# Optimization experiments

Hardware: AMD Instinct MI355X
Metric: run time of the kernel (lower is better)

## Reference

```python
import jax, jax.numpy as jnp
import numpy as np

B, S, F, H = 2, 2048, 2048, 16
DH = F // H  # head_dim = 128
ROPE_BASE = 10000.0


def apply_rope(x, offset):
    # x: [B, S, H, Dh]; rotate-half RoPE per head with positions offset..offset+S-1
    d = x.shape[-1]
    pos = jnp.arange(x.shape[1], dtype=jnp.float32) + offset          # [S]
    inv_freq = 1.0 / (ROPE_BASE ** (jnp.arange(0, d, 2, dtype=jnp.float32) / d))  # [Dh/2]
    ang = pos[:, None] * inv_freq[None, :]                             # [S, Dh/2]
    cos = jnp.cos(ang)[None, :, None, :].astype(x.dtype)               # [1,S,1,Dh/2]
    sin = jnp.sin(ang)[None, :, None, :].astype(x.dtype)
    x1, x2 = x[..., : d // 2], x[..., d // 2 :]
    return jnp.concatenate([x1 * cos - x2 * sin, x1 * sin + x2 * cos], axis=-1)


def setup_inputs() -> dict:
    key = jax.random.key(0)
    k0, k1, k2, k3 = jax.random.split(key, 4)
    lecun = (1.0 / F) ** 0.5
    in_q = jax.random.normal(k0, (B, S, F), dtype=jnp.float32)
    Wq = jax.random.normal(k1, (F, H, DH), dtype=jnp.float32) * lecun
    Wk = jax.random.normal(k2, (F, H, DH), dtype=jnp.float32) * lecun
    Wv = jax.random.normal(k3, (F, H, DH), dtype=jnp.float32) * lecun
    bq = jnp.zeros((H, DH), dtype=jnp.float32)
    bk = jnp.zeros((H, DH), dtype=jnp.float32)
    bv = jnp.zeros((H, DH), dtype=jnp.float32)
    mask = jnp.tril(jnp.ones((S, S), dtype=bool))[None, None, :, :]  # causal [1,1,S,S]
    return {"in_q": in_q, "Wq": Wq, "bq": bq, "Wk": Wk, "bk": bk,
            "Wv": Wv, "bv": bv, "mask": mask, "offset": 0}


def reference(in_q, Wq, bq, Wk, bk, Wv, bv, mask, offset):
    # QKV projections: LinearGeneral [B,S,F] x [F,H,Dh] -> [B,S,H,Dh]
    q = jnp.einsum("bsf,fhd->bshd", in_q, Wq) + bq
    k = jnp.einsum("bsf,fhd->bshd", in_q, Wk) + bk
    v = jnp.einsum("bsf,fhd->bshd", in_q, Wv) + bv
    # RoPE on q and k (merge/split-head reshape in original is a no-op on values)
    q = apply_rope(q, offset)
    k = apply_rope(k, offset)
    # dot-product attention
    scale = 1.0 / jnp.sqrt(jnp.asarray(DH, dtype=q.dtype))
    scores = jnp.einsum("bqhd,bkhd->bhqk", q, k) * scale   # [B,H,Sq,Skv]
    scores = jnp.where(mask, scores, jnp.finfo(scores.dtype).min)
    weights = jax.nn.softmax(scores, axis=-1)
    out = jnp.einsum("bhqk,bkhd->bqhd", weights, v)        # [B,S,H,Dh]
    return out.reshape(out.shape[0], out.shape[1], H * DH)  # merge heads
```

## Files before the change

### kernel.cpp

```cpp
#include <hip/hip_runtime.h>
#include <hip/hip_bf16.h>
#include <stdint.h>

#define NB 2
#define NS 2048
#define NFE 2048
#define NH 16
#define NDH 128

#define QSCALE (0.08838834764831845f * 1.4426950408889634f)

typedef __attribute__((ext_vector_type(4))) float f32x4;
typedef __attribute__((ext_vector_type(8))) __bf16 bf16x8;

__device__ __forceinline__ uint16_t f2bf(float f) {
  uint32_t u = __builtin_bit_cast(uint32_t, f);
  return (uint16_t)((u + 0x7fffu + ((u >> 16) & 1u)) >> 16);
}

__device__ __forceinline__ void gload_lds16(const void* g, void* l) {
  __builtin_amdgcn_global_load_lds((const __attribute__((address_space(1))) void*)g,
                                   (__attribute__((address_space(3))) void*)l,
                                   16, 0, 0);
}

#define MFMA16(a, b, c) __builtin_amdgcn_mfma_f32_16x16x32_bf16(a, b, c, 0, 0, 0)

__global__ void k_convert(const float* __restrict__ x, uint16_t* __restrict__ y) {
  int i = (blockIdx.x * 256 + threadIdx.x) * 4;
  float4 v = *(const float4*)(x + i);
  ushort4 o;
  o.x = f2bf(v.x); o.y = f2bf(v.y); o.z = f2bf(v.z); o.w = f2bf(v.w);
  *(ushort4*)(y + i) = o;
}

__global__ void k_wt(const float* __restrict__ Wq, const float* __restrict__ Wk,
                     const float* __restrict__ Wv, uint16_t* __restrict__ Wt) {
  int which = blockIdx.z;
  const float* Wsrc = (which == 0) ? Wq : ((which == 1) ? Wk : Wv);
  int k0 = blockIdx.x * 64, n0 = blockIdx.y * 64;
  __shared__ uint16_t tile[64][65];
  int t = threadIdx.x;
#pragma unroll
  for (int it = 0; it < 4; ++it) {
    int vec = t + it * 256;
    int r = vec >> 4, c4 = vec & 15;
    float4 v = *(const float4*)&Wsrc[(size_t)(k0 + r) * NFE + n0 + c4 * 4];
    tile[r][c4 * 4 + 0] = f2bf(v.x);
    tile[r][c4 * 4 + 1] = f2bf(v.y);
    tile[r][c4 * 4 + 2] = f2bf(v.z);
    tile[r][c4 * 4 + 3] = f2bf(v.w);
  }
  __syncthreads();
#pragma unroll
  for (int it = 0; it < 4; ++it) {
    int vec = t + it * 256;
    int r = vec >> 4, c4 = vec & 15;
    ushort4 o;
    o.x = tile[c4 * 4 + 0][r];
    o.y = tile[c4 * 4 + 1][r];
    o.z = tile[c4 * 4 + 2][r];
    o.w = tile[c4 * 4 + 3][r];
    *(ushort4*)&Wt[(size_t)which * NFE * NFE + (size_t)(n0 + r) * NFE + k0 + c4 * 4] = o;
  }
}

__global__ void k_rope_tab(float* __restrict__ cosT, float* __restrict__ sinT,
                           const int* __restrict__ offp) {
  int tid = blockIdx.x * 256 + threadIdx.x;
  int s = tid >> 6, i = tid & 63;
  float off = (float)offp[0];
  float inv = expf(-((float)i / 64.0f) * logf(10000.0f));
  float ang = ((float)s + off) * inv;
  cosT[tid] = cosf(ang);
  sinT[tid] = sinf(ang);
}

__global__ __launch_bounds__(512, 2) void k_gemm_qkv(
    const uint16_t* __restrict__ A, const uint16_t* __restrict__ Wt,
    const float* __restrict__ bq, const float* __restrict__ bk, const float* __restrict__ bv,
    const float* __restrict__ cosT, const float* __restrict__ sinT,
    uint16_t* __restrict__ qws, uint16_t* __restrict__ kws, uint16_t* __restrict__ vws) {
  __shared__ uint16_t SMEM[4][16384];

  int bid = blockIdx.x;
  int swzb = (bid & 7) * 48 + (bid >> 3);
  int bx = swzb & 15, by = swzb >> 4;
  int t = threadIdx.x, l = t & 63, w = t >> 6;
  int g = l >> 4, c = l & 15;
  int wr = w >> 1, wc = w & 1;

  int row0 = t >> 3;
  int swz = ((t & 7) ^ (row0 & 7)) << 3;
  const uint16_t* aTh = A + ((size_t)bx * 256 + row0) * NFE + swz;
  const uint16_t* bTh = Wt + ((size_t)by * 256 + row0) * NFE + swz;

#define STG(sbase, slot, h, kt)                                                   \
  do {                                                                            \
    const uint16_t* _s = (sbase) + (size_t)((h) * 128) * NFE + (size_t)(kt) * 64; \
    char* _d = (char*)(&SMEM[slot][0]) + (h) * 16384 + t * 16;                    \
    gload_lds16(_s, _d);                                                          \
    gload_lds16(_s + (size_t)64 * NFE, _d + 8192);                                \
  } while (0)

#define LDA_(buf, mh)                                                             \
  _Pragma("unroll") for (int mi = 0; mi < 2; ++mi)                                \
  _Pragma("unroll") for (int kk = 0; kk < 2; ++kk) {                              \
    int row = wr * 64 + ((mh) * 2 + mi) * 16 + c;                                 \
    af[mi][kk] = *(const bf16x8*)((const char*)SMEM[(buf) * 2] + row * 128 +      \
                                  (((kk * 4 + g) ^ (row & 7)) << 4));             \
  }

#define LDB_(buf, nh, BF)                                                         \
  _Pragma("unroll") for (int ni = 0; ni < 4; ++ni)                                \
  _Pragma("unroll") for (int kk = 0; kk < 2; ++kk) {                              \
    int row = wc * 128 + ((nh) * 4 + ni) * 16 + c;                                \
    BF[ni][kk] = *(const bf16x8*)((const char*)SMEM[(buf) * 2 + 1] + row * 128 +  \
                                  (((kk * 4 + g) ^ (row & 7)) << 4));             \
  }

#define MM_(mh, nh, BF)                                                           \
  _Pragma("unroll") for (int kk = 0; kk < 2; ++kk)                                \
  _Pragma("unroll") for (int mi = 0; mi < 2; ++mi)                                \
  _Pragma("unroll") for (int ni = 0; ni < 4; ++ni)                                \
    acc[(mh) * 2 + mi][(nh) * 4 + ni] =                                           \
        MFMA16(af[mi][kk], BF[ni][kk], acc[(mh) * 2 + mi][(nh) * 4 + ni]);

#define BAR_MID()                                          \
  do {                                                     \
    __builtin_amdgcn_s_barrier();                          \
    asm volatile("s_waitcnt lgkmcnt(0)" ::: "memory");     \
    __builtin_amdgcn_sched_barrier(0);                     \
    __builtin_amdgcn_s_setprio(1);                         \
  } while (0)
#define BAR_END()                                          \
  do {                                                     \
    __builtin_amdgcn_s_setprio(0);                         \
    __builtin_amdgcn_s_barrier();                          \
  } while (0)

  f32x4 acc[4][8];
#pragma unroll
  for (int m = 0; m < 4; ++m)
#pragma unroll
    for (int n = 0; n < 8; ++n) acc[m][n] = (f32x4){0.f, 0.f, 0.f, 0.f};

  bf16x8 af[2][2], bflo[4][2], bfhi[4][2];

  STG(aTh, 0, 0, 0); STG(aTh, 0, 1, 0); STG(bTh, 1, 0, 0); STG(bTh, 1, 1, 0);
  STG(aTh, 2, 0, 1); STG(aTh, 2, 1, 1); STG(bTh, 3, 0, 1); STG(bTh, 3, 1, 1);
  asm volatile("s_waitcnt vmcnt(8)" ::: "memory");
  __builtin_amdgcn_s_barrier();

  for (int i = 0; i < 15; ++i) {
    int t2 = 2 * i + 2, t3 = 2 * i + 3;
    LDA_(0, 0); LDB_(0, 0, bflo);
    BAR_MID(); MM_(0, 0, bflo); BAR_END();
    LDB_(0, 1, bfhi);
    BAR_MID(); MM_(0, 1, bfhi); BAR_END();
    LDA_(0, 1);
    STG(bTh, 1, 0, t2);
    BAR_MID(); MM_(1, 1, bfhi); BAR_END();
    STG(bTh, 1, 1, t2);
    asm volatile("s_waitcnt vmcnt(4)" ::: "memory");
    BAR_MID(); MM_(1, 0, bflo); BAR_END();
    LDA_(1, 0); LDB_(1, 0, bflo);
    STG(aTh, 0, 0, t2);
    BAR_MID(); MM_(0, 0, bflo); BAR_END();
    LDB_(1, 1, bfhi);
    STG(aTh, 0, 1, t2);
    BAR_MID(); MM_(0, 1, bfhi); BAR_END();
    LDA_(1, 1);
    STG(bTh, 3, 0, t3);
    BAR_MID(); MM_(1, 1, bfhi); BAR_END();
    STG(bTh, 3, 1, t3);
    STG(aTh, 2, 0, t3);
    STG(aTh, 2, 1, t3);
    asm volatile("s_waitcnt vmcnt(8)" ::: "memory");
    BAR_MID(); MM_(1, 0, bflo); BAR_END();
  }

  {
    LDA_(0, 0); LDB_(0, 0, bflo);
    BAR_MID(); MM_(0, 0, bflo); BAR_END();
    LDB_(0, 1, bfhi);
    BAR_MID(); MM_(0, 1, bfhi); BAR_END();
    LDA_(0, 1);
    BAR_MID(); MM_(1, 1, bfhi); BAR_END();
    asm volatile("s_waitcnt vmcnt(0)" ::: "memory");
    BAR_MID(); MM_(1, 0, bflo); BAR_END();
    LDA_(1, 0); LDB_(1, 0, bflo);
    BAR_MID(); MM_(0, 0, bflo); BAR_END();
    LDB_(1, 1, bfhi);
    BAR_MID(); MM_(0, 1, bfhi); BAR_END();
    LDA_(1, 1);
    BAR_MID(); MM_(1, 1, bfhi); BAR_END();
    BAR_MID(); MM_(1, 0, bflo); BAR_END();
  }

  int ghead = by * 2 + wc;
  int which = ghead >> 4, h = ghead & 15;
  const float* bias = (which == 0) ? bq : ((which == 1) ? bk : bv);
  uint16_t* outp = (which == 0) ? qws : ((which == 1) ? kws : vws);
  float scl = (which == 0) ? QSCALE : 1.0f;
  int mbase = bx * 256 + wr * 64;
  if (which < 2) {
#pragma unroll
    for (int m = 0; m < 4; ++m)
#pragma unroll
      for (int nf = 0; nf < 4; ++nf) {
        int i2 = nf * 16 + c;
        float b1 = bias[h * NDH + i2], b2 = bias[h * NDH + 64 + i2];
#pragma unroll
        for (int j = 0; j < 4; ++j) {
          int r = mbase + m * 16 + g * 4 + j;
          int bb = r >> 11, s = r & (NS - 1);
          float cs = cosT[(s << 6) + i2], sn = sinT[(s << 6) + i2];
          float x1 = acc[m][nf][j] + b1;
          float x2 = acc[m][nf + 4][j] + b2;
          uint16_t* op = outp + ((size_t)(bb * NH + h) * NS + s) * NDH;
          op[i2] = f2bf((x1 * cs - x2 * sn) * scl);
          op[64 + i2] = f2bf((x1 * sn + x2 * cs) * scl);
        }
      }
  } else {
#pragma unroll
    for (int m = 0; m < 4; ++m)
#pragma unroll
      for (int nf = 0; nf < 8; ++nf) {
        int d = nf * 16 + c;
        float bv_ = bias[h * NDH + d];
#pragma unroll
        for (int j = 0; j < 4; ++j) {
          int r = mbase + m * 16 + g * 4 + j;
          int bb = r >> 11, s = r & (NS - 1);
          outp[((size_t)(bb * NH + h) * NS + s) * NDH + d] = f2bf(acc[m][nf][j] + bv_);
        }
      }
  }
#undef STG
#undef LDA_
#undef LDB_
#undef MM_
#undef BAR_MID
#undef BAR_END
}

__global__ void k_vt(const uint16_t* __restrict__ v, uint16_t* __restrict__ vt) {
  int bh = blockIdx.z;
  int s0 = blockIdx.x * 64, d0 = blockIdx.y * 64;
  __shared__ uint16_t tile[64][65];
  int t = threadIdx.x;
#pragma unroll
  for (int it = 0; it < 4; ++it) {
    int vec = t + it * 256;
    int r = vec >> 4, c4 = vec & 15;
    ushort4 x = *(const ushort4*)&v[((size_t)bh * NS + s0 + r) * NDH + d0 + c4 * 4];
    tile[r][c4 * 4 + 0] = x.x;
    tile[r][c4 * 4 + 1] = x.y;
    tile[r][c4 * 4 + 2] = x.z;
    tile[r][c4 * 4 + 3] = x.w;
  }
  __syncthreads();
#pragma unroll
  for (int it = 0; it < 4; ++it) {
    int vec = t + it * 256;
    int r = vec >> 4, c4 = vec & 15;
    ushort4 o;
    o.x = tile[c4 * 4 + 0][r];
    o.y = tile[c4 * 4 + 1][r];
    o.z = tile[c4 * 4 + 2][r];
    o.w = tile[c4 * 4 + 3][r];
    *(ushort4*)&vt[((size_t)bh * NDH + d0 + r) * NS + s0 + c4 * 4] = o;
  }
}

__global__ __launch_bounds__(256, 4) void k_attn(
    const uint16_t* __restrict__ qws, const uint16_t* __restrict__ kws,
    const uint16_t* __restrict__ vtws, float* __restrict__ out) {
  __shared__ alignas(16) uint16_t Ksm[64 * 128];
  __shared__ alignas(16) uint16_t Vsm[128 * 64];
  __shared__ alignas(16) uint16_t Psm[4][16 * 64];

  int bh = blockIdx.x;
  int t = threadIdx.x, w = t >> 6, l = t & 63;
  int g = l >> 4, c = l & 15;
  int bb = bh >> 4, h = bh & 15;

  const uint16_t* Qp = qws + (size_t)bh * NS * NDH;
  const uint16_t* Kp = kws + (size_t)bh * NS * NDH;
  const uint16_t* Vp = vtws + (size_t)bh * NDH * NS;

  for (int pass = 0; pass < 2; ++pass) {
    int y64 = pass ? (31 - blockIdx.y) : blockIdx.y;
    int q0 = y64 * 64;
    int r = q0 + w * 16 + c;

    bf16x8 qf[4];
#pragma unroll
    for (int kk = 0; kk < 4; ++kk)
      qf[kk] = *(const bf16x8*)&Qp[(size_t)r * NDH + kk * 32 + g * 8];

    f32x4 acc_o[8];
    float mreg = -1e30f, lreg = 0.f;
#pragma unroll
    for (int n = 0; n < 8; ++n) acc_o[n] = (f32x4){0.f, 0.f, 0.f, 0.f};

    int nkt = y64 + 1;
    for (int kt = 0; kt < nkt; ++kt) {
#pragma unroll
      for (int cc = 0; cc < 4; ++cc) {
        int flat = cc * 256 + t;
        int row = flat >> 4, sub = flat & 15;
        int scol = ((sub ^ (row & 7)) << 3);
        gload_lds16(&Kp[(size_t)(kt * 64 + row) * NDH + scol], (char*)Ksm + flat * 16);
      }
#pragma unroll
      for (int cc = 0; cc < 4; ++cc) {
        int flat = cc * 256 + t;
        int row = flat >> 3, sub = flat & 7;
        int scol = ((sub ^ (row & 7)) << 3);
        gload_lds16(&Vp[(size_t)row * NS + kt * 64 + scol], (char*)Vsm + flat * 16);
      }
      __syncthreads();

      f32x4 sacc[4];
#pragma unroll
      for (int nf = 0; nf < 4; ++nf) sacc[nf] = (f32x4){0.f, 0.f, 0.f, 0.f};
#pragma unroll
      for (int kk = 0; kk < 4; ++kk) {
#pragma unroll
        for (int nf = 0; nf < 4; ++nf) {
          int row = nf * 16 + c;
          int kb = ((kk * 32 + g * 8) * 2) ^ ((row & 7) << 4);
          bf16x8 kfr = *(const bf16x8*)((const char*)Ksm + row * 256 + kb);
          sacc[nf] = MFMA16(kfr, qf[kk], sacc[nf]);
        }
      }

      if (kt == y64) {
#pragma unroll
        for (int nf = 0; nf < 4; ++nf)
#pragma unroll
          for (int j = 0; j < 4; ++j) {
            int kv = kt * 64 + nf * 16 + g * 4 + j;
            if (kv > r) sacc[nf][j] = -1e30f;
          }
      }

      float mx = -1e30f;
#pragma unroll
      for (int nf = 0; nf < 4; ++nf)
        mx = fmaxf(mx, fmaxf(fmaxf(sacc[nf][0], sacc[nf][1]),
                             fmaxf(sacc[nf][2], sacc[nf][3])));
      mx = fmaxf(mx, __shfl_xor(mx, 16));
      mx = fmaxf(mx, __shfl_xor(mx, 32));

      float mnew = mreg;
      if (!__all(mx <= mreg + 8.0f)) {
        mnew = fmaxf(mreg, mx);
        float alpha = exp2f(mreg - mnew);
        mreg = mnew;
        lreg *= alpha;
#pragma unroll
        for (int j = 0; j < 4; ++j) {
          float aj = __shfl(alpha, (l & 48) + g * 4 + j);
#pragma unroll
          for (int nf = 0; nf < 8; ++nf) acc_o[nf][j] *= aj;
        }
      }

      float rs = 0.f;
#pragma unroll
      for (int nf = 0; nf < 4; ++nf)
#pragma unroll
        for (int j = 0; j < 4; ++j) {
          float p = exp2f(sacc[nf][j] - mnew);
          sacc[nf][j] = p;
          rs += p;
        }
      rs += __shfl_xor(rs, 16);
      rs += __shfl_xor(rs, 32);
      lreg += rs;

#pragma unroll
      for (int nf = 0; nf < 4; ++nf) {
        uint32_t pk0 = (uint32_t)f2bf(sacc[nf][0]) | ((uint32_t)f2bf(sacc[nf][1]) << 16);
        uint32_t pk1 = (uint32_t)f2bf(sacc[nf][2]) | ((uint32_t)f2bf(sacc[nf][3]) << 16);
        int colb = (nf * 16 + g * 4) * 2;
        char* base = (char*)Psm[w] + c * 128;
        *(uint32_t*)(base + (colb ^ ((c & 7) << 4))) = pk0;
        *(uint32_t*)(base + ((colb + 4) ^ ((c & 7) << 4))) = pk1;
      }

#pragma unroll
      for (int kk2 = 0; kk2 < 2; ++kk2) {
        int prow = c;
        int pkb = ((kk2 * 32 + g * 8) * 2) ^ ((prow & 7) << 4);
        bf16x8 pf = *(const bf16x8*)((const char*)Psm[w] + prow * 128 + pkb);
#pragma unroll
        for (int nf = 0; nf < 8; ++nf) {
          int row = nf * 16 + c;
          int kb = ((kk2 * 32 + g * 8) * 2) ^ ((row & 7) << 4);
          bf16x8 vf = *(const bf16x8*)((const char*)Vsm + row * 128 + kb);
          acc_o[nf] = MFMA16(pf, vf, acc_o[nf]);
        }
      }
      __syncthreads();
    }

#pragma unroll
    for (int j = 0; j < 4; ++j) {
      float lj = __shfl(lreg, (l & 48) + g * 4 + j);
      float inv = 1.0f / lj;
      int s = q0 + w * 16 + g * 4 + j;
      float* op = out + ((size_t)(bb * NS + s)) * NFE + h * NDH;
#pragma unroll
      for (int nf = 0; nf < 8; ++nf) op[nf * 16 + c] = acc_o[nf][j] * inv;
    }
  }
}

extern "C" void kernel_launch(void* const* d_in, const int* in_sizes, int n_in,
                              void* d_out, int out_size, void* d_ws, size_t ws_size,
                              hipStream_t stream) {
  const float* in_q = (const float*)d_in[0];
  const float* Wq = (const float*)d_in[1];
  const float* bq = (const float*)d_in[2];
  const float* Wk = (const float*)d_in[3];
  const float* bk = (const float*)d_in[4];
  const float* Wv = (const float*)d_in[5];
  const float* bv = (const float*)d_in[6];
  const int* offp = (const int*)d_in[8];
  float* out = (float*)d_out;

  char* ws = (char*)d_ws;
  const size_t SZ_AQ = (size_t)4096 * 2048 * 2;
  const size_t SZ_WT = (size_t)3 * 2048 * 2048 * 2;
  const size_t SZ_TAB = (size_t)2048 * 64 * 4;
  const size_t SZ_QKV = (size_t)32 * 2048 * 128 * 2;
  uint16_t* Aq = (uint16_t*)(ws);
  uint16_t* Wt = (uint16_t*)(ws + SZ_AQ);
  float* cosT = (float*)(ws + SZ_AQ + SZ_WT);
  float* sinT = (float*)(ws + SZ_AQ + SZ_WT + SZ_TAB);
  uint16_t* qws = (uint16_t*)(ws + SZ_AQ + SZ_WT + 2 * SZ_TAB);
  uint16_t* kws = (uint16_t*)(ws + SZ_AQ + SZ_WT + 2 * SZ_TAB + SZ_QKV);
  uint16_t* vws = (uint16_t*)(ws + SZ_AQ + SZ_WT + 2 * SZ_TAB + 2 * SZ_QKV);
  uint16_t* vtws = (uint16_t*)(ws + SZ_AQ + SZ_WT + 2 * SZ_TAB + 3 * SZ_QKV);

  k_convert<<<8192, 256, 0, stream>>>(in_q, Aq);
  k_wt<<<dim3(32, 32, 3), 256, 0, stream>>>(Wq, Wk, Wv, Wt);
  k_rope_tab<<<512, 256, 0, stream>>>(cosT, sinT, offp);
  k_gemm_qkv<<<384, 512, 0, stream>>>(Aq, Wt, bq, bk, bv, cosT, sinT, qws, kws, vws);
  k_vt<<<dim3(32, 2, 32), 256, 0, stream>>>(vws, vtws);
  k_attn<<<dim3(32, 16), 256, 0, stream>>>(qws, kws, vtws, out);
}
```

Baseline: 227.9 us.

## Shrink QKV GEMM M-tile to 128 with three-stage LDS pipeline

The QKV projection GEMM tile changes from 256x256 to 128x256, doubling the grid from 384 to 768 blocks. The double-buffered LDS layout becomes a three-slot ring, each slot holding one 64-wide K step of A and B, with a restructured per-K-tile schedule and adjusted vmcnt waits. The aim is better load balance across the CUs, since 384 blocks gives poor wave quantization, and deeper prefetch. The cost is lower arithmetic intensity per block, because B tiles are re-read twice as often.

```diff
diff --git a/kernel.cpp b/kernel.cpp
--- a/kernel.cpp
+++ b/kernel.cpp
@@ -81,50 +81,54 @@
     const float* __restrict__ bq, const float* __restrict__ bk, const float* __restrict__ bv,
     const float* __restrict__ cosT, const float* __restrict__ sinT,
     uint16_t* __restrict__ qws, uint16_t* __restrict__ kws, uint16_t* __restrict__ vws) {
-  __shared__ uint16_t SMEM[4][16384];
+  __shared__ uint16_t SMEM[3][24576];
 
   int bid = blockIdx.x;
-  int swzb = (bid & 7) * 48 + (bid >> 3);
-  int bx = swzb & 15, by = swzb >> 4;
+  int swzb = (bid & 7) * 96 + (bid >> 3);
+  int bx = swzb & 31, by = swzb >> 5;
   int t = threadIdx.x, l = t & 63, w = t >> 6;
   int g = l >> 4, c = l & 15;
   int wr = w >> 1, wc = w & 1;
 
   int row0 = t >> 3;
   int swz = ((t & 7) ^ (row0 & 7)) << 3;
-  const uint16_t* aTh = A + ((size_t)bx * 256 + row0) * NFE + swz;
+  const uint16_t* aTh = A + ((size_t)bx * 128 + row0) * NFE + swz;
   const uint16_t* bTh = Wt + ((size_t)by * 256 + row0) * NFE + swz;
 
-#define STG(sbase, slot, h, kt)                                                   \
-  do {                                                                            \
-    const uint16_t* _s = (sbase) + (size_t)((h) * 128) * NFE + (size_t)(kt) * 64; \
-    char* _d = (char*)(&SMEM[slot][0]) + (h) * 16384 + t * 16;                    \
-    gload_lds16(_s, _d);                                                          \
-    gload_lds16(_s + (size_t)64 * NFE, _d + 8192);                                \
+#define STG_A01B0(slot, u)                                   \
+  do {                                                       \
+    const uint16_t* _a = aTh + (size_t)(u) * 64;             \
+    const uint16_t* _b = bTh + (size_t)(u) * 64;             \
+    char* _d = (char*)(&SMEM[slot][0]) + t * 16;             \
+    gload_lds16(_a, _d);                                     \
+    gload_lds16(_a + (size_t)64 * NFE, _d + 8192);           \
+    gload_lds16(_b, _d + 16384);                             \
   } while (0)
-
-#define LDA_(buf, mh)                                                             \
+#define STG_B123(slot, u)                                    \
+  do {                                                       \
+    const uint16_t* _b = bTh + (size_t)(u) * 64;             \
+    char* _d = (char*)(&SMEM[slot][0]) + t * 16;             \
+    gload_lds16(_b + (size_t)64 * NFE, _d + 24576);          \
+    gload_lds16(_b + (size_t)128 * NFE, _d + 32768);         \
+    gload_lds16(_b + (size_t)192 * NFE, _d + 40960);         \
+  } while (0)
+
+#define LDA_(rb, ks)                                                              \
+  _Pragma("unroll") for (int mi = 0; mi < 2; ++mi) {                              \
+    int row = wr * 32 + mi * 16 + c;                                              \
+    af[mi] = *(const bf16x8*)((const char*)SMEM[rb] + row * 128 +                 \
+                              ((((ks) * 4 + g) ^ (row & 7)) << 4));               \
+  }
+#define LDB_(rb, ks)                                                              \
+  _Pragma("unroll") for (int nf = 0; nf < 8; ++nf) {                              \
+    int row = wc * 128 + nf * 16 + c;                                             \
+    bf[nf] = *(const bf16x8*)((const char*)SMEM[rb] + 16384 + row * 128 +         \
+                              ((((ks) * 4 + g) ^ (row & 7)) << 4));               \
+  }
+#define MM_()                                                                     \
   _Pragma("unroll") for (int mi = 0; mi < 2; ++mi)                                \
-  _Pragma("unroll") for (int kk = 0; kk < 2; ++kk) {                              \
-    int row = wr * 64 + ((mh) * 2 + mi) * 16 + c;                                 \
-    af[mi][kk] = *(const bf16x8*)((const char*)SMEM[(buf) * 2] + row * 128 +      \
-                                  (((kk * 4 + g) ^ (row & 7)) << 4));             \
-  }
-
-#define LDB_(buf, nh, BF)                                                         \
-  _Pragma("unroll") for (int ni = 0; ni < 4; ++ni)                                \
-  _Pragma("unroll") for (int kk = 0; kk < 2; ++kk) {                              \
-    int row = wc * 128 + ((nh) * 4 + ni) * 16 + c;                                \
-    BF[ni][kk] = *(const bf16x8*)((const char*)SMEM[(buf) * 2 + 1] + row * 128 +  \
-                                  (((kk * 4 + g) ^ (row & 7)) << 4));             \
-  }
-
-#define MM_(mh, nh, BF)                                                           \
-  _Pragma("unroll") for (int kk = 0; kk < 2; ++kk)                                \
-  _Pragma("unroll") for (int mi = 0; mi < 2; ++mi)                                \
-  _Pragma("unroll") for (int ni = 0; ni < 4; ++ni)                                \
-    acc[(mh) * 2 + mi][(nh) * 4 + ni] =                                           \
-        MFMA16(af[mi][kk], BF[ni][kk], acc[(mh) * 2 + mi][(nh) * 4 + ni]);
+  _Pragma("unroll") for (int nf = 0; nf < 8; ++nf)                                \
+    acc[mi][nf] = MFMA16(af[mi], bf[nf], acc[mi][nf]);
 
 #define BAR_MID()                                          \
   do {                                                     \
@@ -138,64 +142,49 @@
     __builtin_amdgcn_s_setprio(0);                         \
     __builtin_amdgcn_s_barrier();                          \
   } while (0)
-
-  f32x4 acc[4][8];
-#pragma unroll
-  for (int m = 0; m < 4; ++m)
+#define VM6 asm volatile("s_waitcnt vmcnt(6)" ::: "memory")
+
+#define KTILE(rb, sb, u)                                   \
+  do {                                                     \
+    LDA_(rb, 0); LDB_(rb, 0);                              \
+    STG_A01B0(sb, u);                                      \
+    BAR_MID(); MM_(); BAR_END();                           \
+    LDA_(rb, 1); LDB_(rb, 1);                              \
+    STG_B123(sb, u);                                       \
+    VM6;                                                   \
+    BAR_MID(); MM_(); BAR_END();                           \
+  } while (0)
+
+  f32x4 acc[2][8];
+#pragma unroll
+  for (int m = 0; m < 2; ++m)
 #pragma unroll
     for (int n = 0; n < 8; ++n) acc[m][n] = (f32x4){0.f, 0.f, 0.f, 0.f};
 
-  bf16x8 af[2][2], bflo[4][2], bfhi[4][2];
-
-  STG(aTh, 0, 0, 0); STG(aTh, 0, 1, 0); STG(bTh, 1, 0, 0); STG(bTh, 1, 1, 0);
-  STG(aTh, 2, 0, 1); STG(aTh, 2, 1, 1); STG(bTh, 3, 0, 1); STG(bTh, 3, 1, 1);
-  asm volatile("s_waitcnt vmcnt(8)" ::: "memory");
+  bf16x8 af[2], bf[8];
+
+  STG_A01B0(0, 0); STG_B123(0, 0);
+  STG_A01B0(1, 1); STG_B123(1, 1);
+  VM6;
   __builtin_amdgcn_s_barrier();
 
-  for (int i = 0; i < 15; ++i) {
-    int t2 = 2 * i + 2, t3 = 2 * i + 3;
-    LDA_(0, 0); LDB_(0, 0, bflo);
-    BAR_MID(); MM_(0, 0, bflo); BAR_END();
-    LDB_(0, 1, bfhi);
-    BAR_MID(); MM_(0, 1, bfhi); BAR_END();
-    LDA_(0, 1);
-    STG(bTh, 1, 0, t2);
-    BAR_MID(); MM_(1, 1, bfhi); BAR_END();
-    STG(bTh, 1, 1, t2);
-    asm volatile("s_waitcnt vmcnt(4)" ::: "memory");
-    BAR_MID(); MM_(1, 0, bflo); BAR_END();
-    LDA_(1, 0); LDB_(1, 0, bflo);
-    STG(aTh, 0, 0, t2);
-    BAR_MID(); MM_(0, 0, bflo); BAR_END();
-    LDB_(1, 1, bfhi);
-    STG(aTh, 0, 1, t2);
-    BAR_MID(); MM_(0, 1, bfhi); BAR_END();
-    LDA_(1, 1);
-    STG(bTh, 3, 0, t3);
-    BAR_MID(); MM_(1, 1, bfhi); BAR_END();
-    STG(bTh, 3, 1, t3);
-    STG(aTh, 2, 0, t3);
-    STG(aTh, 2, 1, t3);
-    asm volatile("s_waitcnt vmcnt(8)" ::: "memory");
-    BAR_MID(); MM_(1, 0, bflo); BAR_END();
+  for (int i = 0; i < 10; ++i) {
+    int u0 = 3 * i + 2, u1 = 3 * i + 3, u2 = 3 * i + 4;
+    KTILE(0, 2, u0);
+    KTILE(1, 0, u1);
+    KTILE(2, 1, u2);
   }
 
   {
-    LDA_(0, 0); LDB_(0, 0, bflo);
-    BAR_MID(); MM_(0, 0, bflo); BAR_END();
-    LDB_(0, 1, bfhi);
-    BAR_MID(); MM_(0, 1, bfhi); BAR_END();
-    LDA_(0, 1);
-    BAR_MID(); MM_(1, 1, bfhi); BAR_END();
+    LDA_(0, 0); LDB_(0, 0);
+    BAR_MID(); MM_(); BAR_END();
+    LDA_(0, 1); LDB_(0, 1);
     asm volatile("s_waitcnt vmcnt(0)" ::: "memory");
-    BAR_MID(); MM_(1, 0, bflo); BAR_END();
-    LDA_(1, 0); LDB_(1, 0, bflo);
-    BAR_MID(); MM_(0, 0, bflo); BAR_END();
-    LDB_(1, 1, bfhi);
-    BAR_MID(); MM_(0, 1, bfhi); BAR_END();
-    LDA_(1, 1);
-    BAR_MID(); MM_(1, 1, bfhi); BAR_END();
-    BAR_MID(); MM_(1, 0, bflo); BAR_END();
+    BAR_MID(); MM_(); BAR_END();
+    LDA_(1, 0); LDB_(1, 0);
+    BAR_MID(); MM_(); BAR_END();
+    LDA_(1, 1); LDB_(1, 1);
+    BAR_MID(); MM_(); BAR_END();
   }
 
   int ghead = by * 2 + wc;
@@ -203,10 +192,10 @@
   const float* bias = (which == 0) ? bq : ((which == 1) ? bk : bv);
   uint16_t* outp = (which == 0) ? qws : ((which == 1) ? kws : vws);
   float scl = (which == 0) ? QSCALE : 1.0f;
-  int mbase = bx * 256 + wr * 64;
+  int mbase = bx * 128 + wr * 32;
   if (which < 2) {
 #pragma unroll
-    for (int m = 0; m < 4; ++m)
+    for (int m = 0; m < 2; ++m)
 #pragma unroll
       for (int nf = 0; nf < 4; ++nf) {
         int i2 = nf * 16 + c;
@@ -225,7 +214,7 @@
       }
   } else {
 #pragma unroll
-    for (int m = 0; m < 4; ++m)
+    for (int m = 0; m < 2; ++m)
 #pragma unroll
       for (int nf = 0; nf < 8; ++nf) {
         int d = nf * 16 + c;
@@ -238,12 +227,15 @@
         }
       }
   }
-#undef STG
+#undef STG_A01B0
+#undef STG_B123
 #undef LDA_
 #undef LDB_
 #undef MM_
 #undef BAR_MID
 #undef BAR_END
+#undef VM6
+#undef KTILE
 }
 
 __global__ void k_vt(const uint16_t* __restrict__ v, uint16_t* __restrict__ vt) {
@@ -451,7 +443,7 @@
   k_convert<<<8192, 256, 0, stream>>>(in_q, Aq);
   k_wt<<<dim3(32, 32, 3), 256, 0, stream>>>(Wq, Wk, Wv, Wt);
   k_rope_tab<<<512, 256, 0, stream>>>(cosT, sinT, offp);
-  k_gemm_qkv<<<384, 512, 0, stream>>>(Aq, Wt, bq, bk, bv, cosT, sinT, qws, kws, vws);
+  k_gemm_qkv<<<768, 512, 0, stream>>>(Aq, Wt, bq, bk, bv, cosT, sinT, qws, kws, vws);
   k_vt<<<dim3(32, 2, 32), 256, 0, stream>>>(vws, vtws);
   k_attn<<<dim3(32, 16), 256, 0, stream>>>(qws, kws, vtws, out);
 }
```

Result: faster. 216.6 us (-5.0%).
